# Optimization experiments

Measured on AMD Instinct MI355X. Metric: run time of the kernel, lower is better.

Reference implementation:

```python
import jax, jax.numpy as jnp
from jax import lax
import numpy as np

DIM = 8          # per-head dim
BN_EPS = 1e-5
ATT_EPS = 1e-15


def setup_inputs() -> dict:
    key = jax.random.key(0)
    ks = jax.random.split(key, 6)
    B, C, H, W = 2, 512, 128, 128
    total_dim = 512                      # heads(64) * dim(8)
    c3 = 3 * total_dim                   # 1536
    x = jax.random.normal(ks[0], (B, C, H, W), dtype=jnp.float32)
    w_qkv = jax.random.normal(ks[1], (c3, C), dtype=jnp.float32) * 0.02
    w_dw = jax.random.normal(ks[2], (c3, 1, 5, 5), dtype=jnp.float32) * 0.05
    w_pw = jax.random.normal(ks[3], (c3, 8, 1, 1), dtype=jnp.float32) * 0.1
    w_proj = jax.random.normal(ks[4], (512, 2 * total_dim), dtype=jnp.float32) * 0.02
    bn_gamma = jnp.ones((512,), jnp.float32)
    bn_beta = jnp.zeros((512,), jnp.float32)
    bn_mean = jnp.zeros((512,), jnp.float32)
    bn_var = jnp.ones((512,), jnp.float32)
    return {"x": x, "w_qkv": w_qkv, "w_dw": w_dw, "w_pw": w_pw, "w_proj": w_proj,
            "bn_gamma": bn_gamma, "bn_beta": bn_beta, "bn_mean": bn_mean, "bn_var": bn_var}


def reference(x, w_qkv, w_dw, w_pw, w_proj, bn_gamma, bn_beta, bn_mean, bn_var):
    B, C, H, W = x.shape
    dn = ('NCHW', 'OIHW', 'NCHW')
    # qkv: 1x1 conv, no bias/norm/act
    qkv = jnp.einsum('bchw,oc->bohw', x, w_qkv)  # (B, 1536, H, W)
    # multi-scale aggregation: 5x5 depthwise + 1x1 grouped (groups = 3*heads = 192)
    y = lax.conv_general_dilated(qkv, w_dw, (1, 1), [(2, 2), (2, 2)],
                                 feature_group_count=w_dw.shape[0], dimension_numbers=dn)
    y = lax.conv_general_dilated(y, w_pw, (1, 1), [(0, 0), (0, 0)],
                                 feature_group_count=w_pw.shape[0] // w_pw.shape[1],
                                 dimension_numbers=dn)
    mqkv = jnp.concatenate([qkv, y], axis=1)  # (B, 3072, H, W)
    N = H * W
    mqkv = mqkv.reshape(B, -1, 3 * DIM, N)    # (B, 128 heads, 24, N)
    q = jax.nn.relu(mqkv[:, :, :DIM])          # (B, h, d, N)
    k = jax.nn.relu(mqkv[:, :, DIM:2 * DIM])   # (B, h, d, N)
    v = mqkv[:, :, 2 * DIM:]                   # (B, h, d, N)
    v = jnp.pad(v, ((0, 0), (0, 0), (0, 1), (0, 0)), constant_values=1.0)  # (B,h,d+1,N)
    vk = jnp.einsum('bhdn,bhen->bhde', v, k)   # v @ k^T : (B,h,d+1,d)
    out = jnp.einsum('bhde,bhen->bhdn', vk, q)  # (B,h,d+1,N)
    out = out[:, :, :-1] / (out[:, :, -1:] + ATT_EPS)  # (B,h,d,N)
    out = out.reshape(B, -1, H, W)             # (B, 1024, H, W)
    # proj: 1x1 conv + bn2d (inference-mode affine), no act
    out = jnp.einsum('bchw,oc->bohw', out, w_proj)
    inv = bn_gamma / jnp.sqrt(bn_var + BN_EPS)
    out = out * inv[None, :, None, None] + (bn_beta - bn_mean * inv)[None, :, None, None]
    return out
```

## Files before the change

kernel.cpp:

```cpp
#include <hip/hip_runtime.h>

typedef __bf16 bf16_t;
typedef __bf16 bf16x8 __attribute__((ext_vector_type(8)));
typedef __bf16 bf16x4 __attribute__((ext_vector_type(4)));
typedef __bf16 bf16x2 __attribute__((ext_vector_type(2)));
typedef float  f32x4  __attribute__((ext_vector_type(4)));

#define DEVINL __device__ __forceinline__

static constexpr size_t N_PIX = 16384;

static constexpr size_t OFF_QB  = 0;
static constexpr size_t SZ_QB   = (size_t)512 * N_PIX * 2;
static constexpr size_t OFF_QR  = OFF_QB + SZ_QB;
static constexpr size_t SZ_QR   = SZ_QB;
static constexpr size_t OFF_KV  = OFF_QR + SZ_QR;
static constexpr size_t SZ_KV   = (size_t)1024 * N_PIX * 2;
static constexpr size_t OFF_Y   = OFF_KV + SZ_KV;
static constexpr size_t SZ_Y    = (size_t)1536 * N_PIX * 2;
static constexpr size_t OFF_ATT = OFF_Y + SZ_Y;
static constexpr size_t SZ_ATT  = (size_t)N_PIX * 1024 * 2;
static constexpr size_t OFF_XTH = OFF_ATT;
static constexpr size_t OFF_XTL = OFF_ATT + (size_t)N_PIX * 512 * 2;
static constexpr size_t OFF_WQA = OFF_ATT + SZ_ATT;
static constexpr size_t SZ_WQA  = (size_t)512 * 1536 * 2;
static constexpr size_t OFF_WKV = OFF_WQA + SZ_WQA;
static constexpr size_t SZ_WKV  = (size_t)1024 * 512 * 2;
static constexpr size_t OFF_WP  = OFF_WKV + SZ_WKV;
static constexpr size_t SZ_WP   = (size_t)512 * 1024 * 2;
static constexpr size_t OFF_VK  = OFF_WP + SZ_WP;
static constexpr size_t SZ_VK   = (size_t)128 * 72 * 4;
static constexpr size_t OFF_VKP = OFF_VK + SZ_VK;
static constexpr size_t SZ_VKP  = (size_t)128 * 8 * 72 * 4;
static constexpr size_t OFF_BNA = OFF_VKP + SZ_VKP;
static constexpr size_t OFF_ZP  = OFF_BNA + 2048;
static constexpr size_t WS_NEEDED = OFF_ZP + 64;

DEVINL void gload16(const bf16_t* g, bf16_t* l) {
  __builtin_amdgcn_global_load_lds((const __attribute__((address_space(1))) void*)g,
                                   (__attribute__((address_space(3))) void*)l, 16, 0, 0);
}

__global__ __launch_bounds__(256)
void xpose_kernel(const float* __restrict__ x, bf16_t* __restrict__ xTh, bf16_t* __restrict__ xTl) {
  __shared__ float t[32][33];
  const int n0 = blockIdx.x * 32, c0 = blockIdx.y * 32;
  const int tx = threadIdx.x & 31, ty = threadIdx.x >> 5;
#pragma unroll
  for (int r = 0; r < 4; ++r)
    t[ty + r * 8][tx] = x[(size_t)(c0 + ty + r * 8) * N_PIX + n0 + tx];
  __syncthreads();
  const int nl = threadIdx.x >> 3, sub = threadIdx.x & 7;
  const int c8 = (sub & 3) * 8, plane = sub >> 2;
  bf16x8 o;
#pragma unroll
  for (int k = 0; k < 8; ++k) {
    const float v = t[c8 + k][nl];
    if (plane == 0) {
      o[k] = (bf16_t)v;
    } else {
      const bf16_t hi = (bf16_t)v;
      o[k] = (bf16_t)(v - (float)hi);
    }
  }
  bf16_t* dst = plane ? xTl : xTh;
  *(bf16x8*)&dst[(size_t)(n0 + nl) * 512 + c0 + c8] = o;
}

static constexpr int PREP_W1 = 512 * 1536;
static constexpr int PREP_W2 = 1024 * 512;
static constexpr int PREP_W3 = 512 * 1024;
static constexpr int PREP_TOT = PREP_W1 + PREP_W2 + PREP_W3 + 512 + 16;
__global__ __launch_bounds__(256)
void prep_kernel(const float* __restrict__ wq, const float* __restrict__ wp,
                 const float* __restrict__ gam, const float* __restrict__ bet,
                 const float* __restrict__ mu, const float* __restrict__ va,
                 bf16_t* __restrict__ wqA, bf16_t* __restrict__ wkv, bf16_t* __restrict__ wpb,
                 float* __restrict__ bna, float* __restrict__ zp) {
  const int i = blockIdx.x * 256 + threadIdx.x;
  if (i < PREP_W1) {
    const int r = i / 1536, c = i - r * 1536;
    const int o = (r >> 3) * 24 + (r & 7);
    bf16_t out;
    if (c < 512) {
      out = (bf16_t)wq[o * 512 + c];
    } else if (c < 1024) {
      const float v = wq[o * 512 + c - 512];
      const bf16_t hi = (bf16_t)v;
      out = (bf16_t)(v - (float)hi);
    } else {
      out = (bf16_t)wq[o * 512 + c - 1024];
    }
    wqA[i] = out;
  } else if (i < PREP_W1 + PREP_W2) {
    const int j = i - PREP_W1;
    const int r = j >> 9, c = j & 511;
    const int h = (r & 511) >> 3;
    const int jj = (r < 512 ? 8 : 16) + (r & 7);
    wkv[j] = (bf16_t)wq[(h * 24 + jj) * 512 + c];
  } else if (i < PREP_W1 + PREP_W2 + PREP_W3) {
    const int j = i - PREP_W1 - PREP_W2;
    const int m = j >> 10;
    const float inv = gam[m] / sqrtf(va[m] + 1e-5f);
    wpb[j] = (bf16_t)(wp[j] * inv);
  } else if (i < PREP_W1 + PREP_W2 + PREP_W3 + 512) {
    const int k = i - PREP_W1 - PREP_W2 - PREP_W3;
    const float inv = gam[k] / sqrtf(va[k] + 1e-5f);
    bna[k] = bet[k] - mu[k] * inv;
  } else if (i < PREP_TOT) {
    zp[i - (PREP_W1 + PREP_W2 + PREP_W3 + 512)] = 0.f;
  }
}

__global__ __launch_bounds__(256, 4)
void gemm_qkv_kernel(const bf16_t* __restrict__ wqA, const bf16_t* __restrict__ wkv,
                     const bf16_t* __restrict__ xTh, const bf16_t* __restrict__ xTl,
                     bf16_t* __restrict__ Qb, bf16_t* __restrict__ Qr, bf16_t* __restrict__ KV) {
  __shared__ __align__(16) bf16_t As[128 * 64];
  __shared__ __align__(16) bf16_t Bs[128 * 64];
  const int tid = threadIdx.x, wid = tid >> 6, lane = tid & 63;
  const int fr = lane & 15, fg = lane >> 4;
  const int wm = (wid >> 1) * 64, wn = (wid & 1) * 64;
  const int by = blockIdx.y;
  const bool isQ = by < 4;
  const int m0 = (isQ ? by : by - 4) * 128;
  const int n0 = blockIdx.x * 128;
  const int KA = isQ ? 1536 : 512;
  const bf16_t* Aptr = isQ ? wqA + (size_t)m0 * 1536 : wkv + (size_t)m0 * 512;
  const int srow = tid >> 3;
  const int soff = (((tid & 7) ^ (srow & 7)) * 8);

  f32x4 acc[4][4] = {};

  for (int kk = 0; kk < KA; kk += 64) {
    const bf16_t* Bpl;
    int bcol;
    if (isQ) {
      Bpl  = (kk < 1024) ? xTh : xTl;
      bcol = (kk < 1024) ? (kk & 511) : (kk - 1024);
    } else {
      Bpl = xTh; bcol = kk;
    }
    __syncthreads();
#pragma unroll
    for (int r = 0; r < 4; ++r) {
      gload16(Aptr + (size_t)(srow + 32 * r) * KA + kk + soff, As + (wid * 8 + 32 * r) * 64);
      gload16(Bpl + (size_t)(n0 + srow + 32 * r) * 512 + bcol + soff, Bs + (wid * 8 + 32 * r) * 64);
    }
    __syncthreads();
#pragma unroll
    for (int ks = 0; ks < 2; ++ks) {
      bf16x8 af[4], bfr[4];
#pragma unroll
      for (int i = 0; i < 4; ++i)
        af[i]  = *(const bf16x8*)&As[(wm + i * 16 + fr) * 64 + (((ks * 4 + fg) ^ (fr & 7)) * 8)];
#pragma unroll
      for (int j = 0; j < 4; ++j)
        bfr[j] = *(const bf16x8*)&Bs[(wn + j * 16 + fr) * 64 + (((ks * 4 + fg) ^ (fr & 7)) * 8)];
#pragma unroll
      for (int i = 0; i < 4; ++i)
#pragma unroll
        for (int j = 0; j < 4; ++j)
          acc[i][j] = __builtin_amdgcn_mfma_f32_16x16x32_bf16(af[i], bfr[j], acc[i][j], 0, 0, 0);
    }
  }

#pragma unroll
  for (int i = 0; i < 4; ++i)
#pragma unroll
    for (int r = 0; r < 4; ++r) {
      const int m = m0 + wm + i * 16 + fg * 4 + r;
#pragma unroll
      for (int j = 0; j < 4; ++j) {
        const int n = n0 + wn + j * 16 + fr;
        const float v = acc[i][j][r];
        if (isQ) {
          Qb[(size_t)m * N_PIX + n] = (bf16_t)v;
          Qr[(size_t)m * N_PIX + n] = (bf16_t)fmaxf(0.f, v);
        } else {
          KV[(size_t)m * N_PIX + n] = (bf16_t)v;
        }
      }
    }
}

__global__ __launch_bounds__(256, 4)
void gemm_proj_kernel(const bf16_t* __restrict__ A, const bf16_t* __restrict__ B,
                      float* __restrict__ Cout, const float* __restrict__ bna) {
  __shared__ __align__(16) bf16_t As[128 * 64];
  __shared__ __align__(16) bf16_t Bs[128 * 64];
  const int tid = threadIdx.x, wid = tid >> 6, lane = tid & 63;
  const int fr = lane & 15, fg = lane >> 4;
  const int wm = (wid >> 1) * 64, wn = (wid & 1) * 64;
  const int m0 = blockIdx.y * 128, n0 = blockIdx.x * 128;
  const int srow = tid >> 3;
  const int soff = (((tid & 7) ^ (srow & 7)) * 8);
  const bf16_t* Ab = A + (size_t)m0 * 1024;
  const bf16_t* Bb = B + (size_t)n0 * 1024;

  f32x4 acc[4][4] = {};

  for (int kk = 0; kk < 1024; kk += 64) {
    __syncthreads();
#pragma unroll
    for (int r = 0; r < 4; ++r) {
      gload16(Ab + (size_t)(srow + 32 * r) * 1024 + kk + soff, As + (wid * 8 + 32 * r) * 64);
      gload16(Bb + (size_t)(srow + 32 * r) * 1024 + kk + soff, Bs + (wid * 8 + 32 * r) * 64);
    }
    __syncthreads();
#pragma unroll
    for (int ks = 0; ks < 2; ++ks) {
      bf16x8 af[4], bfr[4];
#pragma unroll
      for (int i = 0; i < 4; ++i)
        af[i]  = *(const bf16x8*)&As[(wm + i * 16 + fr) * 64 + (((ks * 4 + fg) ^ (fr & 7)) * 8)];
#pragma unroll
      for (int j = 0; j < 4; ++j)
        bfr[j] = *(const bf16x8*)&Bs[(wn + j * 16 + fr) * 64 + (((ks * 4 + fg) ^ (fr & 7)) * 8)];
#pragma unroll
      for (int i = 0; i < 4; ++i)
#pragma unroll
        for (int j = 0; j < 4; ++j)
          acc[i][j] = __builtin_amdgcn_mfma_f32_16x16x32_bf16(af[i], bfr[j], acc[i][j], 0, 0, 0);
    }
  }

#pragma unroll
  for (int i = 0; i < 4; ++i)
#pragma unroll
    for (int r = 0; r < 4; ++r) {
      const int m = m0 + wm + i * 16 + fg * 4 + r;
      const float sh = bna[m];
#pragma unroll
      for (int j = 0; j < 4; ++j)
        Cout[(size_t)m * N_PIX + n0 + wn + j * 16 + fr] = acc[i][j][r] + sh;
    }
}

__global__ __launch_bounds__(256)
void dwpw_kernel(const bf16_t* __restrict__ Qb, const bf16_t* __restrict__ KV,
                 const float* __restrict__ wdw, const float* __restrict__ wpw,
                 const bf16_t* __restrict__ zp, bf16_t* __restrict__ y) {
  const int g = blockIdx.y, t = blockIdx.x;
  const int typ = g % 3, head = g / 3;
  const int ty0 = (t >> 1) * 16, tx0 = (t & 1) * 64;
  const int tid = threadIdx.x, wid = tid >> 6, lane = tid & 63;
  __shared__ __align__(16) bf16_t sin_[8][20][80];
  __shared__ float swd[8][25];
  __shared__ float swp[8][8];
  if (tid < 200) swd[tid / 25][tid % 25] = wdw[(g * 8 + tid / 25) * 25 + tid % 25];
  if (tid < 64)  swp[tid >> 3][tid & 7] = wpw[(g * 8 + (tid >> 3)) * 8 + (tid & 7)];
  const bf16_t* plane = (typ == 0) ? (Qb + (size_t)head * 8 * N_PIX)
                                   : (KV + (size_t)((typ == 2 ? 512 : 0) + head * 8) * N_PIX);
  bf16_t* sflat = &sin_[0][0][0];
  for (int base = wid * 64; base < 1600; base += 256) {
    const int id  = base + lane;
    const int ch  = id / 200;
    const int rem = id - ch * 200;
    const int row = rem / 10;
    const int c6  = rem - row * 10;
    const int gy  = ty0 + row - 2;
    const int gx  = tx0 + c6 * 8 - 8;
    const bool ok = ((unsigned)gy < 128u) && ((unsigned)gx < 128u);
    const bf16_t* src = ok ? (plane + (size_t)ch * N_PIX + gy * 128 + gx) : zp;
    gload16(src, sflat + (size_t)base * 8);
  }
  __syncthreads();

  const int px4 = (tid & 15) * 4, py = tid >> 4;
  float dwres[8][4];
#pragma unroll
  for (int ch = 0; ch < 8; ++ch) {
    float o0 = 0.f, o1 = 0.f, o2 = 0.f, o3 = 0.f;
#pragma unroll
    for (int di = 0; di < 5; ++di) {
      bf16x4 a0 = *(const bf16x4*)&sin_[ch][py + di][px4 + 4];
      bf16x4 a1 = *(const bf16x4*)&sin_[ch][py + di][px4 + 8];
      bf16x4 a2 = *(const bf16x4*)&sin_[ch][py + di][px4 + 12];
      float vv[12] = {(float)a0[0], (float)a0[1], (float)a0[2], (float)a0[3],
                      (float)a1[0], (float)a1[1], (float)a1[2], (float)a1[3],
                      (float)a2[0], (float)a2[1], (float)a2[2], (float)a2[3]};
#pragma unroll
      for (int dj = 0; dj < 5; ++dj) {
        const float w = swd[ch][di * 5 + dj];
        o0 += vv[dj + 2] * w; o1 += vv[dj + 3] * w;
        o2 += vv[dj + 4] * w; o3 += vv[dj + 5] * w;
      }
    }
    dwres[ch][0] = o0; dwres[ch][1] = o1; dwres[ch][2] = o2; dwres[ch][3] = o3;
  }
#pragma unroll
  for (int oc = 0; oc < 8; ++oc) {
    float o[4] = {0.f, 0.f, 0.f, 0.f};
#pragma unroll
    for (int ic = 0; ic < 8; ++ic) {
      const float w = swp[oc][ic];
#pragma unroll
      for (int u = 0; u < 4; ++u) o[u] += dwres[ic][u] * w;
    }
    bf16x4 ov;
#pragma unroll
    for (int u = 0; u < 4; ++u) ov[u] = (bf16_t)o[u];
    *(bf16x4*)&y[(size_t)(8 * g + oc) * N_PIX + (ty0 + py) * 128 + tx0 + px4] = ov;
  }
}

__global__ __launch_bounds__(256)
void vk_partial_kernel(const bf16_t* __restrict__ KV, const bf16_t* __restrict__ yb,
                       float* __restrict__ part) {
  const int h = blockIdx.y, s = blockIdx.x;
  const bf16_t *kb, *vb;
  if (h < 64) {
    kb = KV + (size_t)(h * 8) * N_PIX;
    vb = KV + (size_t)(512 + h * 8) * N_PIX;
  } else {
    kb = yb + (size_t)(24 * (h - 64) + 8) * N_PIX;
    vb = yb + (size_t)(24 * (h - 64) + 16) * N_PIX;
  }
  float a[8][8] = {};
  float ak[8] = {};
  const int p0 = s * 2048 + (int)threadIdx.x * 8;
  float kq[8][8], vq[8][8];
#pragma unroll
  for (int e = 0; e < 8; ++e) {
    bf16x8 kk = *(const bf16x8*)&kb[(size_t)e * N_PIX + p0];
#pragma unroll
    for (int u = 0; u < 8; ++u) kq[e][u] = fmaxf(0.f, (float)kk[u]);
  }
#pragma unroll
  for (int d = 0; d < 8; ++d) {
    bf16x8 vv = *(const bf16x8*)&vb[(size_t)d * N_PIX + p0];
#pragma unroll
    for (int u = 0; u < 8; ++u) vq[d][u] = (float)vv[u];
  }
#pragma unroll
  for (int d = 0; d < 8; ++d)
#pragma unroll
    for (int e = 0; e < 8; ++e)
#pragma unroll
      for (int u = 0; u < 8; ++u) a[d][e] += vq[d][u] * kq[e][u];
#pragma unroll
  for (int e = 0; e < 8; ++e)
#pragma unroll
    for (int u = 0; u < 8; ++u) ak[e] += kq[e][u];

  __shared__ float red[4][72];
  const int lane = threadIdx.x & 63, wid = threadIdx.x >> 6;
#pragma unroll
  for (int i = 0; i < 72; ++i) {
    float v = (i < 64) ? a[i >> 3][i & 7] : ak[i - 64];
    v += __shfl_xor(v, 32); v += __shfl_xor(v, 16); v += __shfl_xor(v, 8);
    v += __shfl_xor(v, 4);  v += __shfl_xor(v, 2);  v += __shfl_xor(v, 1);
    if (lane == 0) red[wid][i] = v;
  }
  __syncthreads();
  if (threadIdx.x < 72) {
    const float sum_ = red[0][threadIdx.x] + red[1][threadIdx.x] + red[2][threadIdx.x] + red[3][threadIdx.x];
    part[((size_t)h * 8 + s) * 72 + threadIdx.x] = sum_;
  }
}

__global__ __launch_bounds__(128)
void vk_reduce_kernel(const float* __restrict__ part, float* __restrict__ vk) {
  const int h = blockIdx.x;
  const int i = threadIdx.x;
  if (i < 72) {
    float s = 0.f;
#pragma unroll
    for (int t = 0; t < 8; ++t) s += part[((size_t)h * 8 + t) * 72 + i];
    vk[(size_t)h * 72 + i] = s;
  }
}

__global__ __launch_bounds__(256)
void attn_kernel(const bf16_t* __restrict__ Qr, const bf16_t* __restrict__ yb,
                 const float* __restrict__ vk, bf16_t* __restrict__ attT) {
  const int n0 = blockIdx.x * 32;
  const int tid = threadIdx.x;
  const int px = tid & 31, hl = tid >> 5;
  __shared__ __align__(16) bf16_t att_s[32 * 512];
  __shared__ float vk_s[576];
  for (int grp = 0; grp < 2; ++grp) {
    for (int hg = 0; hg < 8; ++hg) {
      __syncthreads();
      for (int i = tid; i < 576; i += 256)
        vk_s[i] = vk[((size_t)grp * 64 + hg * 8) * 72 + i];
      __syncthreads();
      const int hh = hg * 8 + hl;
      float q[8];
      if (grp == 0) {
        const bf16_t* plane = Qr + (size_t)(hh * 8) * N_PIX + n0 + px;
#pragma unroll
        for (int e = 0; e < 8; ++e) q[e] = (float)plane[(size_t)e * N_PIX];
      } else {
        const bf16_t* plane = yb + (size_t)(24 * hh) * N_PIX + n0 + px;
#pragma unroll
        for (int e = 0; e < 8; ++e) q[e] = fmaxf(0.f, (float)plane[(size_t)e * N_PIX]);
      }
      float den = 1e-15f;
#pragma unroll
      for (int e = 0; e < 8; ++e) den += vk_s[hl * 72 + 64 + e] * q[e];
      const float rden = 1.0f / den;
      bf16x8 r8;
#pragma unroll
      for (int d = 0; d < 8; ++d) {
        float num = 0.f;
#pragma unroll
        for (int e = 0; e < 8; ++e) num += vk_s[hl * 72 + d * 8 + e] * q[e];
        r8[d] = (bf16_t)(num * rden);
      }
      const int chunk = hg * 8 + hl;
      *(bf16x8*)&att_s[px * 512 + ((chunk ^ (px & 7)) << 3)] = r8;
    }
    __syncthreads();
    bf16_t* dst = attT + (size_t)n0 * 1024 + grp * 512;
    for (int i = tid; i < 2048; i += 256) {
      const int r = i >> 6, cc = i & 63;
      bf16x8 v = *(const bf16x8*)&att_s[r * 512 + (((cc ^ (r & 7))) << 3)];
      *(bf16x8*)&dst[(size_t)r * 1024 + cc * 8] = v;
    }
  }
}

extern "C" void kernel_launch(void* const* d_in, const int* in_sizes, int n_in,
                              void* d_out, int out_size, void* d_ws, size_t ws_size,
                              hipStream_t stream) {
  if (ws_size < WS_NEEDED) return;
  const float* x      = (const float*)d_in[0];
  const float* w_qkv  = (const float*)d_in[1];
  const float* w_dw   = (const float*)d_in[2];
  const float* w_pw   = (const float*)d_in[3];
  const float* w_proj = (const float*)d_in[4];
  const float* gam    = (const float*)d_in[5];
  const float* bet    = (const float*)d_in[6];
  const float* mu     = (const float*)d_in[7];
  const float* va     = (const float*)d_in[8];

  char* w = (char*)d_ws;
  bf16_t* Qb   = (bf16_t*)(w + OFF_QB);
  bf16_t* Qr   = (bf16_t*)(w + OFF_QR);
  bf16_t* KV   = (bf16_t*)(w + OFF_KV);
  bf16_t* yb   = (bf16_t*)(w + OFF_Y);
  bf16_t* xTh  = (bf16_t*)(w + OFF_XTH);
  bf16_t* xTl  = (bf16_t*)(w + OFF_XTL);
  bf16_t* attT = (bf16_t*)(w + OFF_ATT);
  bf16_t* wqA  = (bf16_t*)(w + OFF_WQA);
  bf16_t* wkv  = (bf16_t*)(w + OFF_WKV);
  bf16_t* wpb  = (bf16_t*)(w + OFF_WP);
  float*  vk   = (float*)(w + OFF_VK);
  float*  part = (float*)(w + OFF_VKP);
  float*  bna  = (float*)(w + OFF_BNA);
  float*  zp   = (float*)(w + OFF_ZP);

  dim3 blk(256);
  prep_kernel<<<dim3((PREP_TOT + 255) / 256), blk, 0, stream>>>(
      w_qkv, w_proj, gam, bet, mu, va, wqA, wkv, wpb, bna, zp);

  for (int b = 0; b < 2; ++b) {
    const float* xb = x + (size_t)b * 512 * N_PIX;
    float* outb = (float*)d_out + (size_t)b * 512 * N_PIX;
    xpose_kernel<<<dim3(512, 16), blk, 0, stream>>>(xb, xTh, xTl);
    gemm_qkv_kernel<<<dim3(128, 12), blk, 0, stream>>>(wqA, wkv, xTh, xTl, Qb, Qr, KV);
    dwpw_kernel<<<dim3(16, 192), blk, 0, stream>>>(Qb, KV, w_dw, w_pw, (const bf16_t*)zp, yb);
    vk_partial_kernel<<<dim3(8, 128), blk, 0, stream>>>(KV, yb, part);
    vk_reduce_kernel<<<dim3(128), dim3(128), 0, stream>>>(part, vk);
    attn_kernel<<<dim3(512), blk, 0, stream>>>(Qr, yb, vk, attT);
    gemm_proj_kernel<<<dim3(128, 4), blk, 0, stream>>>(wpb, attT, outb, bna);
  }
}
```

Baseline: 369.0 us.

## Fold vk into projection weights and switch intermediates to fp16 packed math

The per-head vk matrix is folded into the projection weights by a new w2_kernel (W2 = Wproj·vk per head), so the attention kernel only writes q scaled by the reciprocal denominator instead of computing an 8x8 matvec per pixel. Intermediate Q/KV/y buffers move from bf16 to fp16, and the depthwise/pointwise conv now runs in packed half2 arithmetic with shifted-pair operands. This removes per-pixel attention arithmetic and halves ALU work in dwpw, at the cost of an extra small kernel per batch and reduced accumulation precision (fp16 accumulation in the convs, rounding of the folded weights to bf16).

```diff
diff --git a/kernel.cpp b/kernel.cpp
--- a/kernel.cpp
+++ b/kernel.cpp
@@ -3,8 +3,11 @@
 typedef __bf16 bf16_t;
 typedef __bf16 bf16x8 __attribute__((ext_vector_type(8)));
 typedef __bf16 bf16x4 __attribute__((ext_vector_type(4)));
-typedef __bf16 bf16x2 __attribute__((ext_vector_type(2)));
 typedef float  f32x4  __attribute__((ext_vector_type(4)));
+typedef _Float16 h16;
+typedef _Float16 h16x2 __attribute__((ext_vector_type(2)));
+typedef _Float16 h16x4 __attribute__((ext_vector_type(4)));
+typedef _Float16 h16x8 __attribute__((ext_vector_type(8)));
 
 #define DEVINL __device__ __forceinline__
 
@@ -34,9 +37,11 @@
 static constexpr size_t SZ_VKP  = (size_t)128 * 8 * 72 * 4;
 static constexpr size_t OFF_BNA = OFF_VKP + SZ_VKP;
 static constexpr size_t OFF_ZP  = OFF_BNA + 2048;
-static constexpr size_t WS_NEEDED = OFF_ZP + 64;
-
-DEVINL void gload16(const bf16_t* g, bf16_t* l) {
+static constexpr size_t OFF_W2  = OFF_ZP + 64;
+static constexpr size_t SZ_W2   = (size_t)512 * 1024 * 2;
+static constexpr size_t WS_NEEDED = OFF_W2 + SZ_W2;
+
+DEVINL void gload16(const void* g, void* l) {
   __builtin_amdgcn_global_load_lds((const __attribute__((address_space(1))) void*)g,
                                    (__attribute__((address_space(3))) void*)l, 16, 0, 0);
 }
@@ -115,7 +120,7 @@
 __global__ __launch_bounds__(256, 4)
 void gemm_qkv_kernel(const bf16_t* __restrict__ wqA, const bf16_t* __restrict__ wkv,
                      const bf16_t* __restrict__ xTh, const bf16_t* __restrict__ xTl,
-                     bf16_t* __restrict__ Qb, bf16_t* __restrict__ Qr, bf16_t* __restrict__ KV) {
+                     h16* __restrict__ Qb, h16* __restrict__ Qr, h16* __restrict__ KV) {
   __shared__ __align__(16) bf16_t As[128 * 64];
   __shared__ __align__(16) bf16_t Bs[128 * 64];
   const int tid = threadIdx.x, wid = tid >> 6, lane = tid & 63;
@@ -175,10 +180,10 @@
         const int n = n0 + wn + j * 16 + fr;
         const float v = acc[i][j][r];
         if (isQ) {
-          Qb[(size_t)m * N_PIX + n] = (bf16_t)v;
-          Qr[(size_t)m * N_PIX + n] = (bf16_t)fmaxf(0.f, v);
+          Qb[(size_t)m * N_PIX + n] = (h16)v;
+          Qr[(size_t)m * N_PIX + n] = (h16)fmaxf(0.f, v);
         } else {
-          KV[(size_t)m * N_PIX + n] = (bf16_t)v;
+          KV[(size_t)m * N_PIX + n] = (h16)v;
         }
       }
     }
@@ -238,21 +243,29 @@
 }
 
 __global__ __launch_bounds__(256)
-void dwpw_kernel(const bf16_t* __restrict__ Qb, const bf16_t* __restrict__ KV,
+void dwpw_kernel(const h16* __restrict__ Qb, const h16* __restrict__ KV,
                  const float* __restrict__ wdw, const float* __restrict__ wpw,
-                 const bf16_t* __restrict__ zp, bf16_t* __restrict__ y) {
+                 const h16* __restrict__ zp, h16* __restrict__ y) {
   const int g = blockIdx.y, t = blockIdx.x;
   const int typ = g % 3, head = g / 3;
   const int ty0 = (t >> 1) * 16, tx0 = (t & 1) * 64;
   const int tid = threadIdx.x, wid = tid >> 6, lane = tid & 63;
-  __shared__ __align__(16) bf16_t sin_[8][20][80];
-  __shared__ float swd[8][25];
-  __shared__ float swp[8][8];
-  if (tid < 200) swd[tid / 25][tid % 25] = wdw[(g * 8 + tid / 25) * 25 + tid % 25];
-  if (tid < 64)  swp[tid >> 3][tid & 7] = wpw[(g * 8 + (tid >> 3)) * 8 + (tid & 7)];
-  const bf16_t* plane = (typ == 0) ? (Qb + (size_t)head * 8 * N_PIX)
-                                   : (KV + (size_t)((typ == 2 ? 512 : 0) + head * 8) * N_PIX);
-  bf16_t* sflat = &sin_[0][0][0];
+  __shared__ __align__(16) h16 sin_[8][20][80];
+  __shared__ h16x2 swd2[8][25];
+  __shared__ h16x2 swp2[8][8];
+  if (tid < 200) {
+    const h16 w = (h16)wdw[(g * 8 + tid / 25) * 25 + tid % 25];
+    h16x2 w2; w2[0] = w; w2[1] = w;
+    swd2[tid / 25][tid % 25] = w2;
+  }
+  if (tid < 64) {
+    const h16 w = (h16)wpw[(g * 8 + (tid >> 3)) * 8 + (tid & 7)];
+    h16x2 w2; w2[0] = w; w2[1] = w;
+    swp2[tid >> 3][tid & 7] = w2;
+  }
+  const h16* plane = (typ == 0) ? (Qb + (size_t)head * 8 * N_PIX)
+                                : (KV + (size_t)((typ == 2 ? 512 : 0) + head * 8) * N_PIX);
+  h16* sflat = &sin_[0][0][0];
   for (int base = wid * 64; base < 1600; base += 256) {
     const int id  = base + lane;
     const int ch  = id / 200;
@@ -262,54 +275,57 @@
     const int gy  = ty0 + row - 2;
     const int gx  = tx0 + c6 * 8 - 8;
     const bool ok = ((unsigned)gy < 128u) && ((unsigned)gx < 128u);
-    const bf16_t* src = ok ? (plane + (size_t)ch * N_PIX + gy * 128 + gx) : zp;
+    const h16* src = ok ? (plane + (size_t)ch * N_PIX + gy * 128 + gx) : zp;
     gload16(src, sflat + (size_t)base * 8);
   }
   __syncthreads();
 
   const int px4 = (tid & 15) * 4, py = tid >> 4;
-  float dwres[8][4];
+  h16x2 dwa[8][2];
 #pragma unroll
   for (int ch = 0; ch < 8; ++ch) {
-    float o0 = 0.f, o1 = 0.f, o2 = 0.f, o3 = 0.f;
+    h16x2 A0 = 0, A1 = 0;
 #pragma unroll
     for (int di = 0; di < 5; ++di) {
-      bf16x4 a0 = *(const bf16x4*)&sin_[ch][py + di][px4 + 4];
-      bf16x4 a1 = *(const bf16x4*)&sin_[ch][py + di][px4 + 8];
-      bf16x4 a2 = *(const bf16x4*)&sin_[ch][py + di][px4 + 12];
-      float vv[12] = {(float)a0[0], (float)a0[1], (float)a0[2], (float)a0[3],
-                      (float)a1[0], (float)a1[1], (float)a1[2], (float)a1[3],
-                      (float)a2[0], (float)a2[1], (float)a2[2], (float)a2[3]};
-#pragma unroll
-      for (int dj = 0; dj < 5; ++dj) {
-        const float w = swd[ch][di * 5 + dj];
-        o0 += vv[dj + 2] * w; o1 += vv[dj + 3] * w;
-        o2 += vv[dj + 4] * w; o3 += vv[dj + 5] * w;
-      }
-    }
-    dwres[ch][0] = o0; dwres[ch][1] = o1; dwres[ch][2] = o2; dwres[ch][3] = o3;
+      const uint2 w0 = *(const uint2*)&sin_[ch][py + di][px4 + 4];
+      const uint2 w1 = *(const uint2*)&sin_[ch][py + di][px4 + 8];
+      const uint2 w2v = *(const uint2*)&sin_[ch][py + di][px4 + 12];
+      const unsigned u1 = w0.y, u2 = w1.x, u3 = w1.y, u4 = w2v.x;
+      const h16x2 P2 = __builtin_bit_cast(h16x2, u1);
+      const h16x2 P3 = __builtin_bit_cast(h16x2, (u2 << 16) | (u1 >> 16));
+      const h16x2 P4 = __builtin_bit_cast(h16x2, u2);
+      const h16x2 P5 = __builtin_bit_cast(h16x2, (u3 << 16) | (u2 >> 16));
+      const h16x2 P6 = __builtin_bit_cast(h16x2, u3);
+      const h16x2 P7 = __builtin_bit_cast(h16x2, (u4 << 16) | (u3 >> 16));
+      const h16x2 P8 = __builtin_bit_cast(h16x2, u4);
+      h16x2 wd;
+      wd = swd2[ch][di * 5 + 0]; A0 += wd * P2; A1 += wd * P4;
+      wd = swd2[ch][di * 5 + 1]; A0 += wd * P3; A1 += wd * P5;
+      wd = swd2[ch][di * 5 + 2]; A0 += wd * P4; A1 += wd * P6;
+      wd = swd2[ch][di * 5 + 3]; A0 += wd * P5; A1 += wd * P7;
+      wd = swd2[ch][di * 5 + 4]; A0 += wd * P6; A1 += wd * P8;
+    }
+    dwa[ch][0] = A0; dwa[ch][1] = A1;
   }
 #pragma unroll
   for (int oc = 0; oc < 8; ++oc) {
-    float o[4] = {0.f, 0.f, 0.f, 0.f};
+    h16x2 o0 = 0, o1 = 0;
 #pragma unroll
     for (int ic = 0; ic < 8; ++ic) {
-      const float w = swp[oc][ic];
-#pragma unroll
-      for (int u = 0; u < 4; ++u) o[u] += dwres[ic][u] * w;
-    }
-    bf16x4 ov;
-#pragma unroll
-    for (int u = 0; u < 4; ++u) ov[u] = (bf16_t)o[u];
-    *(bf16x4*)&y[(size_t)(8 * g + oc) * N_PIX + (ty0 + py) * 128 + tx0 + px4] = ov;
-  }
-}
-
-__global__ __launch_bounds__(256)
-void vk_partial_kernel(const bf16_t* __restrict__ KV, const bf16_t* __restrict__ yb,
+      const h16x2 w = swp2[oc][ic];
+      o0 += w * dwa[ic][0];
+      o1 += w * dwa[ic][1];
+    }
+    h16x4 ov; ov[0] = o0[0]; ov[1] = o0[1]; ov[2] = o1[0]; ov[3] = o1[1];
+    *(h16x4*)&y[(size_t)(8 * g + oc) * N_PIX + (ty0 + py) * 128 + tx0 + px4] = ov;
+  }
+}
+
+__global__ __launch_bounds__(256)
+void vk_partial_kernel(const h16* __restrict__ KV, const h16* __restrict__ yb,
                        float* __restrict__ part) {
   const int h = blockIdx.y, s = blockIdx.x;
-  const bf16_t *kb, *vb;
+  const h16 *kb, *vb;
   if (h < 64) {
     kb = KV + (size_t)(h * 8) * N_PIX;
     vb = KV + (size_t)(512 + h * 8) * N_PIX;
@@ -323,13 +339,13 @@
   float kq[8][8], vq[8][8];
 #pragma unroll
   for (int e = 0; e < 8; ++e) {
-    bf16x8 kk = *(const bf16x8*)&kb[(size_t)e * N_PIX + p0];
+    h16x8 kk = *(const h16x8*)&kb[(size_t)e * N_PIX + p0];
 #pragma unroll
     for (int u = 0; u < 8; ++u) kq[e][u] = fmaxf(0.f, (float)kk[u]);
   }
 #pragma unroll
   for (int d = 0; d < 8; ++d) {
-    bf16x8 vv = *(const bf16x8*)&vb[(size_t)d * N_PIX + p0];
+    h16x8 vv = *(const h16x8*)&vb[(size_t)d * N_PIX + p0];
 #pragma unroll
     for (int u = 0; u < 8; ++u) vq[d][u] = (float)vv[u];
   }
@@ -373,47 +389,55 @@
 }
 
 __global__ __launch_bounds__(256)
-void attn_kernel(const bf16_t* __restrict__ Qr, const bf16_t* __restrict__ yb,
-                 const float* __restrict__ vk, bf16_t* __restrict__ attT) {
+void w2_kernel(const bf16_t* __restrict__ wpb, const float* __restrict__ vkm,
+               bf16_t* __restrict__ W2) {
+  const int idx = blockIdx.x * 256 + threadIdx.x;
+  const int m = idx >> 10, c = idx & 1023;
+  const int h = c >> 3, e = c & 7;
+  float s = 0.f;
+#pragma unroll
+  for (int d = 0; d < 8; ++d)
+    s += (float)wpb[(size_t)m * 1024 + h * 8 + d] * vkm[h * 72 + d * 8 + e];
+  W2[idx] = (bf16_t)s;
+}
+
+__global__ __launch_bounds__(256)
+void qn_kernel(const h16* __restrict__ Qr, const h16* __restrict__ yb,
+               const float* __restrict__ vk, bf16_t* __restrict__ qnT) {
   const int n0 = blockIdx.x * 32;
   const int tid = threadIdx.x;
   const int px = tid & 31, hl = tid >> 5;
   __shared__ __align__(16) bf16_t att_s[32 * 512];
-  __shared__ float vk_s[576];
+  __shared__ float ak_s[64];
   for (int grp = 0; grp < 2; ++grp) {
     for (int hg = 0; hg < 8; ++hg) {
       __syncthreads();
-      for (int i = tid; i < 576; i += 256)
-        vk_s[i] = vk[((size_t)grp * 64 + hg * 8) * 72 + i];
+      if (tid < 64)
+        ak_s[tid] = vk[((size_t)grp * 64 + hg * 8 + (tid >> 3)) * 72 + 64 + (tid & 7)];
       __syncthreads();
       const int hh = hg * 8 + hl;
       float q[8];
       if (grp == 0) {
-        const bf16_t* plane = Qr + (size_t)(hh * 8) * N_PIX + n0 + px;
+        const h16* plane = Qr + (size_t)(hh * 8) * N_PIX + n0 + px;
 #pragma unroll
         for (int e = 0; e < 8; ++e) q[e] = (float)plane[(size_t)e * N_PIX];
       } else {
-        const bf16_t* plane = yb + (size_t)(24 * hh) * N_PIX + n0 + px;
+        const h16* plane = yb + (size_t)(24 * hh) * N_PIX + n0 + px;
 #pragma unroll
         for (int e = 0; e < 8; ++e) q[e] = fmaxf(0.f, (float)plane[(size_t)e * N_PIX]);
       }
       float den = 1e-15f;
 #pragma unroll
-      for (int e = 0; e < 8; ++e) den += vk_s[hl * 72 + 64 + e] * q[e];
+      for (int e = 0; e < 8; ++e) den += ak_s[hl * 8 + e] * q[e];
       const float rden = 1.0f / den;
       bf16x8 r8;
 #pragma unroll
-      for (int d = 0; d < 8; ++d) {
-        float num = 0.f;
-#pragma unroll
-        for (int e = 0; e < 8; ++e) num += vk_s[hl * 72 + d * 8 + e] * q[e];
-        r8[d] = (bf16_t)(num * rden);
-      }
+      for (int e = 0; e < 8; ++e) r8[e] = (bf16_t)(q[e] * rden);
       const int chunk = hg * 8 + hl;
       *(bf16x8*)&att_s[px * 512 + ((chunk ^ (px & 7)) << 3)] = r8;
     }
     __syncthreads();
-    bf16_t* dst = attT + (size_t)n0 * 1024 + grp * 512;
+    bf16_t* dst = qnT + (size_t)n0 * 1024 + grp * 512;
     for (int i = tid; i < 2048; i += 256) {
       const int r = i >> 6, cc = i & 63;
       bf16x8 v = *(const bf16x8*)&att_s[r * 512 + (((cc ^ (r & 7))) << 3)];
@@ -437,16 +461,17 @@
   const float* va     = (const float*)d_in[8];
 
   char* w = (char*)d_ws;
-  bf16_t* Qb   = (bf16_t*)(w + OFF_QB);
-  bf16_t* Qr   = (bf16_t*)(w + OFF_QR);
-  bf16_t* KV   = (bf16_t*)(w + OFF_KV);
-  bf16_t* yb   = (bf16_t*)(w + OFF_Y);
+  h16*    Qb   = (h16*)(w + OFF_QB);
+  h16*    Qr   = (h16*)(w + OFF_QR);
+  h16*    KV   = (h16*)(w + OFF_KV);
+  h16*    yb   = (h16*)(w + OFF_Y);
   bf16_t* xTh  = (bf16_t*)(w + OFF_XTH);
   bf16_t* xTl  = (bf16_t*)(w + OFF_XTL);
-  bf16_t* attT = (bf16_t*)(w + OFF_ATT);
+  bf16_t* qnT  = (bf16_t*)(w + OFF_ATT);
   bf16_t* wqA  = (bf16_t*)(w + OFF_WQA);
   bf16_t* wkv  = (bf16_t*)(w + OFF_WKV);
   bf16_t* wpb  = (bf16_t*)(w + OFF_WP);
+  bf16_t* W2   = (bf16_t*)(w + OFF_W2);
   float*  vk   = (float*)(w + OFF_VK);
   float*  part = (float*)(w + OFF_VKP);
   float*  bna  = (float*)(w + OFF_BNA);
@@ -461,10 +486,11 @@
     float* outb = (float*)d_out + (size_t)b * 512 * N_PIX;
     xpose_kernel<<<dim3(512, 16), blk, 0, stream>>>(xb, xTh, xTl);
     gemm_qkv_kernel<<<dim3(128, 12), blk, 0, stream>>>(wqA, wkv, xTh, xTl, Qb, Qr, KV);
-    dwpw_kernel<<<dim3(16, 192), blk, 0, stream>>>(Qb, KV, w_dw, w_pw, (const bf16_t*)zp, yb);
+    dwpw_kernel<<<dim3(16, 192), blk, 0, stream>>>(Qb, KV, w_dw, w_pw, (const h16*)zp, yb);
     vk_partial_kernel<<<dim3(8, 128), blk, 0, stream>>>(KV, yb, part);
     vk_reduce_kernel<<<dim3(128), dim3(128), 0, stream>>>(part, vk);
-    attn_kernel<<<dim3(512), blk, 0, stream>>>(Qr, yb, vk, attT);
-    gemm_proj_kernel<<<dim3(128, 4), blk, 0, stream>>>(wpb, attT, outb, bna);
-  }
-}
+    w2_kernel<<<dim3(512 * 1024 / 256), blk, 0, stream>>>(wpb, vk, W2);
+    qn_kernel<<<dim3(512), blk, 0, stream>>>(Qr, yb, vk, qnT);
+    gemm_proj_kernel<<<dim3(128, 4), blk, 0, stream>>>(W2, qnT, outb, bna);
+  }
+}
```

New measurement: 350.2 us. 5.1% less time.
